# Kernel optimization log

Measured on AMD Instinct MI355X. Metric: run time of the kernel, lower is better.

The kernel has to match this reference:

```python
import jax, jax.numpy as jnp
import numpy as np

EPS = 1e-5

def _layernorm(x, gamma):
    # LayerNorm over last dim, no bias (torch LayerNorm(bias=False))
    mu = jnp.mean(x, axis=-1, keepdims=True)
    var = jnp.mean(jnp.square(x - mu), axis=-1, keepdims=True)
    return (x - mu) * jax.lax.rsqrt(var + EPS) * gamma

def setup_inputs() -> dict:
    B, N, D = 32, 1024, 512
    key = jax.random.key(0)
    ks = jax.random.split(key, 6)
    x = jax.random.normal(ks[0], (B, N, D), dtype=jnp.float32)
    # valid lengths in [1, N] so no query row has all keys masked
    belief_base_sizes = jax.random.randint(ks[1], (B,), 1, N + 1, dtype=jnp.int32)
    s = 0.02
    w_qkv = jax.random.normal(ks[2], (D, 3 * D), dtype=jnp.float32) * s
    w_fc = jax.random.normal(ks[3], (D, D), dtype=jnp.float32) * s
    w_proj = jax.random.normal(ks[4], (D, D), dtype=jnp.float32) * s
    g1 = jnp.ones((D,), dtype=jnp.float32)
    g2 = jnp.ones((D,), dtype=jnp.float32)
    return {"x": x, "belief_base_sizes": belief_base_sizes, "g1": g1,
            "w_qkv": w_qkv, "g2": g2, "w_fc": w_fc, "w_proj": w_proj}

def reference(x, belief_base_sizes, g1, w_qkv, g2, w_fc, w_proj):
    B, N, D = x.shape
    h = _layernorm(x, g1)                      # LN1
    qkv = jnp.einsum('bnd,de->bne', h, w_qkv)  # [B,N,3D]
    q, k, v = jnp.split(qkv, 3, axis=-1)
    scores = jnp.einsum('bqd,bkd->bqk', q, k) / jnp.sqrt(jnp.float32(D))
    # mask key columns >= valid size (rows are NOT masked, matching the original)
    col = jnp.arange(N)
    pad = col[None, None, :] >= belief_base_sizes[:, None, None]  # [B,1,N]
    scores = jnp.where(pad, -jnp.inf, scores)
    attn = jax.nn.softmax(scores, axis=-1)
    y = jnp.einsum('bqk,bkd->bqd', attn, v)
    y = _layernorm(y, g2)                      # LN2 (no residual in original)
    y = jnp.einsum('bnd,de->bne', y, w_fc)
    y = jax.nn.gelu(y, approximate=False)      # torch GELU default = exact erf
    y = jnp.einsum('bnd,de->bne', y, w_proj)
    return y
```

## Files before the change

kernel.cpp:

```cpp
#include <hip/hip_runtime.h>
#include <hip/hip_bf16.h>
#include <cmath>


using f16 = _Float16;
typedef _Float16 f16x8 __attribute__((ext_vector_type(8)));
typedef _Float16 f16x4 __attribute__((ext_vector_type(4)));
typedef _Float16 f16x2 __attribute__((ext_vector_type(2)));
typedef float f32x4 __attribute__((ext_vector_type(4)));

#define NB 32
#define NN 1024
#define ND 512

#define GLOAD_LDS16(g, l)                                                     \
    __builtin_amdgcn_global_load_lds(                                         \
        (const __attribute__((address_space(1))) void*)(g),                   \
        (__attribute__((address_space(3))) void*)(l), 16, 0, 0)

__global__ void transpose_cast_w(const float* __restrict__ w, f16* __restrict__ wT,
                                 int K, int Ncols) {
    __shared__ float tile[32][33];
    const int n0 = blockIdx.x * 32, k0 = blockIdx.y * 32;
    const int tx = threadIdx.x, ty = threadIdx.y;
    for (int i = ty; i < 32; i += 8)
        tile[i][tx] = w[(long long)(k0 + i) * Ncols + n0 + tx];
    __syncthreads();
    for (int i = ty; i < 32; i += 8)
        wT[(long long)(n0 + i) * K + k0 + tx] = (f16)tile[tx][i];
}

template <typename TIN>
__global__ __launch_bounds__(256) void ln_kernel(const TIN* __restrict__ x,
                                                 const float* __restrict__ gamma,
                                                 f16* __restrict__ out) {
    const int tid = threadIdx.x;
    const long long base = (long long)blockIdx.x * ND;
    float v0, v1;
    if constexpr (sizeof(TIN) == 4) {
        const float2 t = ((const float2*)(x + base))[tid];
        v0 = t.x; v1 = t.y;
    } else {
        const f16x2 t = ((const f16x2*)(x + base))[tid];
        v0 = (float)t.x; v1 = (float)t.y;
    }

    __shared__ float red[8];
    const int wave = tid >> 6, lane = tid & 63;

    float s = v0 + v1;
#pragma unroll
    for (int o = 32; o > 0; o >>= 1) s += __shfl_down(s, o, 64);
    if (lane == 0) red[wave] = s;
    __syncthreads();
    const float mean = (red[0] + red[1] + red[2] + red[3]) * (1.f / 512.f);
    __syncthreads();

    const float d0 = v0 - mean, d1 = v1 - mean;
    float q = d0 * d0 + d1 * d1;
#pragma unroll
    for (int o = 32; o > 0; o >>= 1) q += __shfl_down(q, o, 64);
    if (lane == 0) red[wave] = q;
    __syncthreads();
    const float var = (red[0] + red[1] + red[2] + red[3]) * (1.f / 512.f);
    const float rstd = rsqrtf(var + 1e-5f);

    f16x2 o2;
    o2.x = (f16)(d0 * rstd * gamma[2 * tid]);
    o2.y = (f16)(d1 * rstd * gamma[2 * tid + 1]);
    ((f16x2*)(out + base))[tid] = o2;
}

__global__ __launch_bounds__(256) void softmax_wave(f16* __restrict__ scores,
                                                    const int* __restrict__ sizes) {
    const int b = blockIdx.y;
    const int wave = threadIdx.x >> 6, lane = threadIdx.x & 63;
    const int row = blockIdx.x * 4 + wave;
    f16* srow = scores + ((long long)b * NN + row) * NN;
    const int sz = sizes[b];
    const int keff = (sz + 31) & ~31;
    const int cbase = lane * 16;

    const f16x8 a0 = *(const f16x8*)&srow[cbase];
    const f16x8 a1 = *(const f16x8*)&srow[cbase + 8];
    float v[16];
#pragma unroll
    for (int e = 0; e < 8; e++) { v[e] = (float)a0[e]; v[8 + e] = (float)a1[e]; }

    float m = -1e30f;
#pragma unroll
    for (int e = 0; e < 16; e++)
        if (cbase + e < sz) m = fmaxf(m, v[e]);
#pragma unroll
    for (int o = 32; o > 0; o >>= 1) m = fmaxf(m, __shfl_xor(m, o, 64));

    float s = 0.f;
#pragma unroll
    for (int e = 0; e < 16; e++) {
        v[e] = (cbase + e < sz) ? __expf(v[e] - m) : 0.f;
        s += v[e];
    }
#pragma unroll
    for (int o = 32; o > 0; o >>= 1) s += __shfl_xor(s, o, 64);
    const float inv = 1.f / s;

    if (cbase < keff) {
        f16x8 o0, o1;
#pragma unroll
        for (int e = 0; e < 8; e++) {
            o0[e] = (f16)(v[e] * inv);
            o1[e] = (f16)(v[8 + e] * inv);
        }
        *(f16x8*)&srow[cbase] = o0;
        *(f16x8*)&srow[cbase + 8] = o1;
    }
}

__device__ __forceinline__ float gelu_exact(float x) {
    return 0.5f * x * (1.f + erff(x * 0.70710678118654752f));
}

template <int MODE, int MASKN, int MASKK>
__global__ __launch_bounds__(256) void gemm_bt(
    const f16* __restrict__ A, int lda, long long strideA,
    const f16* __restrict__ Bt, int ldb, long long strideB,
    void* __restrict__ Cv, int ldc, long long strideC,
    int K, float alpha, const int* __restrict__ sizes, void* __restrict__ Cv2) {
    __shared__ __align__(16) f16 As[128 * 32];
    __shared__ __align__(16) f16 Bs[128 * 32];

    const int tid = threadIdx.x;
    const int wave = tid >> 6, lane = tid & 63;
    const int wr = (wave >> 1) * 64, wc = (wave & 1) * 64;
    const int lrow = lane & 15, quad = lane >> 4;
    const long long m0 = (long long)blockIdx.y * 128;
    const long long n0 = (long long)blockIdx.x * 128;

    if (MASKN) {
        if (n0 >= sizes[blockIdx.z]) return;
    }
    int Keff = K;
    if (MASKK) {
        const int ke = (sizes[blockIdx.z] + 31) & ~31;
        if (ke < Keff) Keff = ke;
    }

    A += (long long)blockIdx.z * strideA;
    Bt += (long long)blockIdx.z * strideB;

    f32x4 acc[4][4];
#pragma unroll
    for (int i = 0; i < 4; i++)
#pragma unroll
        for (int j = 0; j < 4; j++) acc[i][j] = (f32x4){0.f, 0.f, 0.f, 0.f};

    const int s0 = tid, s1 = tid + 256;
    const int r0 = s0 >> 2, c0 = ((s0 & 3) ^ ((r0 >> 1) & 3)) * 8;
    const int r1 = s1 >> 2, c1 = ((s1 & 3) ^ ((r1 >> 1) & 3)) * 8;

    const f16* Ar0 = A + (m0 + r0) * lda + c0;
    const f16* Ar1 = A + (m0 + r1) * lda + c1;
    const f16* Br0 = Bt + (n0 + r0) * ldb + c0;
    const f16* Br1 = Bt + (n0 + r1) * ldb + c1;

    const int swz8 = (quad ^ ((lrow >> 1) & 3)) * 8;

    for (int k0 = 0; k0 < Keff; k0 += 32) {
        __syncthreads();
        GLOAD_LDS16(Ar0 + k0, &As[s0 * 8]);
        GLOAD_LDS16(Ar1 + k0, &As[s1 * 8]);
        GLOAD_LDS16(Br0 + k0, &Bs[s0 * 8]);
        GLOAD_LDS16(Br1 + k0, &Bs[s1 * 8]);
        __syncthreads();

        f16x8 af[4], bf[4];
#pragma unroll
        for (int i = 0; i < 4; i++)
            af[i] = *(const f16x8*)&As[(wr + i * 16 + lrow) * 32 + swz8];
#pragma unroll
        for (int j = 0; j < 4; j++)
            bf[j] = *(const f16x8*)&Bs[(wc + j * 16 + lrow) * 32 + swz8];
#pragma unroll
        for (int i = 0; i < 4; i++)
#pragma unroll
            for (int j = 0; j < 4; j++)
                acc[i][j] = __builtin_amdgcn_mfma_f32_16x16x32_f16(af[i], bf[j], acc[i][j], 0, 0, 0);
    }

    if (MODE == 3 && n0 >= 1024) {
        f16* vTp = (f16*)Cv2;
#pragma unroll
        for (int i = 0; i < 4; i++) {
            const long long rbase = m0 + wr + i * 16 + quad * 4;
            const long long bb = rbase >> 10;
            const long long nrow = rbase & 1023;
#pragma unroll
            for (int j = 0; j < 4; j++) {
                const long long col = n0 + wc + j * 16 + lrow - 1024;
                f16x4 pk;
#pragma unroll
                for (int r = 0; r < 4; r++) pk[r] = (f16)acc[i][j][r];
                *(f16x4*)&vTp[bb * ND * NN + col * NN + nrow] = pk;
            }
        }
        return;
    }
    float* Cf = (float*)Cv + (long long)blockIdx.z * strideC;
    f16* Ch = (f16*)Cv + (long long)blockIdx.z * strideC;
#pragma unroll
    for (int i = 0; i < 4; i++) {
        const long long rbase = m0 + wr + i * 16 + quad * 4;
#pragma unroll
        for (int j = 0; j < 4; j++) {
            const long long col = n0 + wc + j * 16 + lrow;
#pragma unroll
            for (int r = 0; r < 4; r++) {
                float vv = acc[i][j][r];
                if (MODE == 1) {
                    Cf[(rbase + r) * ldc + col] = vv * alpha;
                } else if (MODE == 2) {
                    Ch[(rbase + r) * ldc + col] = (f16)gelu_exact(vv);
                } else {
                    Ch[(rbase + r) * ldc + col] = (f16)(vv * alpha);
                }
            }
        }
    }
}

extern "C" void kernel_launch(void* const* d_in, const int* in_sizes, int n_in,
                              void* d_out, int out_size, void* d_ws, size_t ws_size,
                              hipStream_t stream) {
    const float* x     = (const float*)d_in[0];
    const int*   sizes = (const int*)d_in[1];
    const float* g1    = (const float*)d_in[2];
    const float* wqkv  = (const float*)d_in[3];
    const float* g2    = (const float*)d_in[4];
    const float* wfc   = (const float*)d_in[5];
    const float* wproj = (const float*)d_in[6];
    float* out = (float*)d_out;
    char* ws = (char*)d_ws;

    f16* wqkvT  = (f16*)(ws + (0ull << 20));
    f16* wfcT   = (f16*)(ws + (2ull << 20));
    f16* wprojT = (f16*)(ws + (3ull << 20));
    f16* qk     = (f16*)(ws + (4ull << 20));
    f16* vT     = (f16*)(ws + (68ull << 20));
    f16* scoreb = (f16*)(ws + (100ull << 20));
    f16* ln2o   = (f16*)(ws + (4ull << 20));
    f16* gelub  = (f16*)(ws + (36ull << 20));

    f16* h = (f16*)d_out;
    f16* y = (f16*)d_out + (long long)NB * NN * ND;

    long long avail = (long long)ws_size - (100ll << 20);
    int CB = (int)(avail / (2ll << 20));
    if (CB < 1) CB = 1;
    if (CB > NB) CB = NB;

    const dim3 t32x8(32, 8);

    transpose_cast_w<<<dim3(48, 16), t32x8, 0, stream>>>(wqkv, wqkvT, 512, 1536);
    transpose_cast_w<<<dim3(16, 16), t32x8, 0, stream>>>(wfc, wfcT, 512, 512);
    transpose_cast_w<<<dim3(16, 16), t32x8, 0, stream>>>(wproj, wprojT, 512, 512);

    ln_kernel<float><<<NB * NN, 256, 0, stream>>>(x, g1, h);

    gemm_bt<3, 0, 0><<<dim3(12, 256, 1), 256, 0, stream>>>(
        h, 512, 0, wqkvT, 512, 0, qk, 1024, 0, 512, 1.0f, nullptr, vT);

    for (int b0 = 0; b0 < NB; b0 += CB) {
        const int nb = (NB - b0) < CB ? (NB - b0) : CB;
        const f16* qc = qk + (long long)b0 * NN * 1024;

        gemm_bt<0, 1, 0><<<dim3(8, 8, nb), 256, 0, stream>>>(
            qc, 1024, (long long)NN * 1024, qc + 512, 1024, (long long)NN * 1024,
            scoreb, 1024, (long long)NN * 1024, 512, 0.044194173824159216f,
            sizes + b0, nullptr);

        softmax_wave<<<dim3(NN / 4, nb), 256, 0, stream>>>(scoreb, sizes + b0);

        gemm_bt<0, 0, 1><<<dim3(4, 8, nb), 256, 0, stream>>>(
            scoreb, 1024, (long long)NN * 1024,
            vT + (long long)b0 * ND * NN, NN, (long long)ND * NN,
            y + (long long)b0 * NN * ND, ND, (long long)NN * ND, NN, 1.0f,
            sizes + b0, nullptr);
    }

    ln_kernel<f16><<<NB * NN, 256, 0, stream>>>(y, g2, ln2o);

    gemm_bt<2, 0, 0><<<dim3(4, 256, 1), 256, 0, stream>>>(
        ln2o, 512, 0, wfcT, 512, 0, gelub, 512, 0, 512, 1.0f, nullptr, nullptr);

    gemm_bt<1, 0, 0><<<dim3(4, 256, 1), 256, 0, stream>>>(
        gelub, 512, 0, wprojT, 512, 0, out, 512, 0, 512, 1.0f, nullptr, nullptr);
}
```

Before: 453.3 us.

## Double GEMM K-tile to 64, merge weight transposes, fix attention batching

The GEMM kernel now stages 64-wide K tiles in LDS with an 8-way XOR swizzle and runs two MFMA sub-steps per barrier pair. This halves the number of synchronisations and doubles the bytes in flight per load phase. The three weight transpose launches become one launch with a z-indexed grid. The attention loop now runs as two fixed 16-batch phases, with score buffers placed in the output buffer and in reused workspace, which replaces the workspace-size-dependent chunking. The softmax and masked-K rounding move to multiples of 64 to match the new tile. The larger LDS footprint may lower occupancy, and the hardcoded buffer aliasing assumes a particular layout.

```diff
diff --git a/kernel.cpp b/kernel.cpp
--- a/kernel.cpp
+++ b/kernel.cpp
@@ -18,8 +18,15 @@
         (const __attribute__((address_space(1))) void*)(g),                   \
         (__attribute__((address_space(3))) void*)(l), 16, 0, 0)
 
-__global__ void transpose_cast_w(const float* __restrict__ w, f16* __restrict__ wT,
-                                 int K, int Ncols) {
+__global__ void transpose_cast_all(const float* __restrict__ wqkv, f16* __restrict__ wqkvT,
+                                   const float* __restrict__ wfc, f16* __restrict__ wfcT,
+                                   const float* __restrict__ wproj, f16* __restrict__ wprojT) {
+    const int z = blockIdx.z;
+    const float* w = (z == 0) ? wqkv : (z == 1) ? wfc : wproj;
+    f16* wT       = (z == 0) ? wqkvT : (z == 1) ? wfcT : wprojT;
+    const int Ncols = (z == 0) ? 1536 : 512;
+    if ((int)blockIdx.x * 32 >= Ncols) return;
+
     __shared__ float tile[32][33];
     const int n0 = blockIdx.x * 32, k0 = blockIdx.y * 32;
     const int tx = threadIdx.x, ty = threadIdx.y;
@@ -27,7 +34,7 @@
         tile[i][tx] = w[(long long)(k0 + i) * Ncols + n0 + tx];
     __syncthreads();
     for (int i = ty; i < 32; i += 8)
-        wT[(long long)(n0 + i) * K + k0 + tx] = (f16)tile[tx][i];
+        wT[(long long)(n0 + i) * 512 + k0 + tx] = (f16)tile[tx][i];
 }
 
 template <typename TIN>
@@ -78,7 +85,7 @@
     const int row = blockIdx.x * 4 + wave;
     f16* srow = scores + ((long long)b * NN + row) * NN;
     const int sz = sizes[b];
-    const int keff = (sz + 31) & ~31;
+    const int keff = (sz + 63) & ~63;
     const int cbase = lane * 16;
 
     const f16x8 a0 = *(const f16x8*)&srow[cbase];
@@ -126,8 +133,8 @@
     const f16* __restrict__ Bt, int ldb, long long strideB,
     void* __restrict__ Cv, int ldc, long long strideC,
     int K, float alpha, const int* __restrict__ sizes, void* __restrict__ Cv2) {
-    __shared__ __align__(16) f16 As[128 * 32];
-    __shared__ __align__(16) f16 Bs[128 * 32];
+    __shared__ __align__(16) f16 As[128 * 64];
+    __shared__ __align__(16) f16 Bs[128 * 64];
 
     const int tid = threadIdx.x;
     const int wave = tid >> 6, lane = tid & 63;
@@ -141,7 +148,7 @@
     }
     int Keff = K;
     if (MASKK) {
-        const int ke = (sizes[blockIdx.z] + 31) & ~31;
+        const int ke = (sizes[blockIdx.z] + 63) & ~63;
         if (ke < Keff) Keff = ke;
     }
 
@@ -154,37 +161,40 @@
 #pragma unroll
         for (int j = 0; j < 4; j++) acc[i][j] = (f32x4){0.f, 0.f, 0.f, 0.f};
 
-    const int s0 = tid, s1 = tid + 256;
-    const int r0 = s0 >> 2, c0 = ((s0 & 3) ^ ((r0 >> 1) & 3)) * 8;
-    const int r1 = s1 >> 2, c1 = ((s1 & 3) ^ ((r1 >> 1) & 3)) * 8;
-
-    const f16* Ar0 = A + (m0 + r0) * lda + c0;
-    const f16* Ar1 = A + (m0 + r1) * lda + c1;
-    const f16* Br0 = Bt + (n0 + r0) * ldb + c0;
-    const f16* Br1 = Bt + (n0 + r1) * ldb + c1;
-
-    const int swz8 = (quad ^ ((lrow >> 1) & 3)) * 8;
-
-    for (int k0 = 0; k0 < Keff; k0 += 32) {
+    const f16* Ap[4];
+    const f16* Bp[4];
+#pragma unroll
+    for (int p = 0; p < 4; p++) {
+        const int s = tid + p * 256;
+        const int r = s >> 3, c = ((s & 7) ^ (r & 7)) * 8;
+        Ap[p] = A + (m0 + r) * lda + c;
+        Bp[p] = Bt + (n0 + r) * ldb + c;
+    }
+
+    for (int k0 = 0; k0 < Keff; k0 += 64) {
         __syncthreads();
-        GLOAD_LDS16(Ar0 + k0, &As[s0 * 8]);
-        GLOAD_LDS16(Ar1 + k0, &As[s1 * 8]);
-        GLOAD_LDS16(Br0 + k0, &Bs[s0 * 8]);
-        GLOAD_LDS16(Br1 + k0, &Bs[s1 * 8]);
+#pragma unroll
+        for (int p = 0; p < 4; p++) GLOAD_LDS16(Ap[p] + k0, &As[(tid + p * 256) * 8]);
+#pragma unroll
+        for (int p = 0; p < 4; p++) GLOAD_LDS16(Bp[p] + k0, &Bs[(tid + p * 256) * 8]);
         __syncthreads();
 
-        f16x8 af[4], bf[4];
-#pragma unroll
-        for (int i = 0; i < 4; i++)
-            af[i] = *(const f16x8*)&As[(wr + i * 16 + lrow) * 32 + swz8];
-#pragma unroll
-        for (int j = 0; j < 4; j++)
-            bf[j] = *(const f16x8*)&Bs[(wc + j * 16 + lrow) * 32 + swz8];
-#pragma unroll
-        for (int i = 0; i < 4; i++)
+#pragma unroll
+        for (int h = 0; h < 2; h++) {
+            const int gq = ((h * 4 + quad) ^ (lrow & 7)) * 8;
+            f16x8 af[4], bf[4];
+#pragma unroll
+            for (int i = 0; i < 4; i++)
+                af[i] = *(const f16x8*)&As[(wr + i * 16 + lrow) * 64 + gq];
 #pragma unroll
             for (int j = 0; j < 4; j++)
-                acc[i][j] = __builtin_amdgcn_mfma_f32_16x16x32_f16(af[i], bf[j], acc[i][j], 0, 0, 0);
+                bf[j] = *(const f16x8*)&Bs[(wc + j * 16 + lrow) * 64 + gq];
+#pragma unroll
+            for (int i = 0; i < 4; i++)
+#pragma unroll
+                for (int j = 0; j < 4; j++)
+                    acc[i][j] = __builtin_amdgcn_mfma_f32_16x16x32_f16(af[i], bf[j], acc[i][j], 0, 0, 0);
+        }
     }
 
     if (MODE == 3 && n0 >= 1024) {
@@ -246,45 +256,41 @@
     f16* wprojT = (f16*)(ws + (3ull << 20));
     f16* qk     = (f16*)(ws + (4ull << 20));
     f16* vT     = (f16*)(ws + (68ull << 20));
-    f16* scoreb = (f16*)(ws + (100ull << 20));
-    f16* ln2o   = (f16*)(ws + (4ull << 20));
-    f16* gelub  = (f16*)(ws + (36ull << 20));
-
-    f16* h = (f16*)d_out;
-    f16* y = (f16*)d_out + (long long)NB * NN * ND;
-
-    long long avail = (long long)ws_size - (100ll << 20);
-    int CB = (int)(avail / (2ll << 20));
-    if (CB < 1) CB = 1;
-    if (CB > NB) CB = NB;
-
-    const dim3 t32x8(32, 8);
-
-    transpose_cast_w<<<dim3(48, 16), t32x8, 0, stream>>>(wqkv, wqkvT, 512, 1536);
-    transpose_cast_w<<<dim3(16, 16), t32x8, 0, stream>>>(wfc, wfcT, 512, 512);
-    transpose_cast_w<<<dim3(16, 16), t32x8, 0, stream>>>(wproj, wprojT, 512, 512);
+    f16* scoresB = (f16*)(ws + (4ull << 20));
+    f16* ln2o   = (f16*)(ws + (36ull << 20));
+    f16* gelub  = (f16*)(ws + (4ull << 20));
+
+    f16* h       = (f16*)d_out;
+    f16* scoresA = (f16*)d_out;
+    f16* y       = (f16*)d_out + (long long)NB * NN * ND;
+
+    const long long sstr = (long long)NN * NN;
+    const long long qstr = (long long)NN * 1024;
+    const long long vstr = (long long)ND * NN;
+    const long long ystr = (long long)NN * ND;
+
+    transpose_cast_all<<<dim3(48, 16, 3), dim3(32, 8), 0, stream>>>(
+        wqkv, wqkvT, wfc, wfcT, wproj, wprojT);
 
     ln_kernel<float><<<NB * NN, 256, 0, stream>>>(x, g1, h);
 
     gemm_bt<3, 0, 0><<<dim3(12, 256, 1), 256, 0, stream>>>(
         h, 512, 0, wqkvT, 512, 0, qk, 1024, 0, 512, 1.0f, nullptr, vT);
 
-    for (int b0 = 0; b0 < NB; b0 += CB) {
-        const int nb = (NB - b0) < CB ? (NB - b0) : CB;
-        const f16* qc = qk + (long long)b0 * NN * 1024;
-
-        gemm_bt<0, 1, 0><<<dim3(8, 8, nb), 256, 0, stream>>>(
-            qc, 1024, (long long)NN * 1024, qc + 512, 1024, (long long)NN * 1024,
-            scoreb, 1024, (long long)NN * 1024, 512, 0.044194173824159216f,
-            sizes + b0, nullptr);
-
-        softmax_wave<<<dim3(NN / 4, nb), 256, 0, stream>>>(scoreb, sizes + b0);
-
-        gemm_bt<0, 0, 1><<<dim3(4, 8, nb), 256, 0, stream>>>(
-            scoreb, 1024, (long long)NN * 1024,
-            vT + (long long)b0 * ND * NN, NN, (long long)ND * NN,
-            y + (long long)b0 * NN * ND, ND, (long long)NN * ND, NN, 1.0f,
-            sizes + b0, nullptr);
+    for (int ph = 0; ph < 2; ph++) {
+        const int b0 = ph * 16;
+        f16* sc = ph ? scoresB : scoresA;
+        const f16* qc = qk + (long long)b0 * qstr;
+
+        gemm_bt<0, 1, 0><<<dim3(8, 8, 16), 256, 0, stream>>>(
+            qc, 1024, qstr, qc + 512, 1024, qstr,
+            sc, NN, sstr, 512, 0.044194173824159216f, sizes + b0, nullptr);
+
+        softmax_wave<<<dim3(NN / 4, 16), 256, 0, stream>>>(sc, sizes + b0);
+
+        gemm_bt<0, 0, 1><<<dim3(4, 8, 16), 256, 0, stream>>>(
+            sc, NN, sstr, vT + (long long)b0 * vstr, NN, vstr,
+            y + (long long)b0 * ystr, ND, ystr, NN, 1.0f, sizes + b0, nullptr);
     }
 
     ln_kernel<f16><<<NB * NN, 256, 0, stream>>>(y, g2, ln2o);
```

Result: no change. 448.2 us (-1.1%).
